# Kernel optimization log

Hardware: AMD Instinct MI355X
Metric: run time of the kernel (lower is better)

## Reference

```python
import math
import jax, jax.numpy as jnp
import numpy as np

B, S, H = 2, 2048, 2048
N_HEADS, N_KV_HEADS = 16, 4
HEAD_DIM = H // N_HEADS  # 128
ROPE_BASE = 10000.0


def setup_inputs() -> dict:
    key = jax.random.key(0)
    ks = jax.random.split(key, 8)
    hidden_states = jax.random.normal(ks[0], (B, S, H), dtype=jnp.float32)
    # continuous, increasing timestamps in [0, S)
    time_values = jnp.sort(jax.random.uniform(ks[1], (B, S), dtype=jnp.float32) * S, axis=-1)
    sc = 1.0 / math.sqrt(H)
    wq = jax.random.normal(ks[2], (H, N_HEADS * HEAD_DIM), dtype=jnp.float32) * sc
    bq = jnp.zeros((N_HEADS * HEAD_DIM,), dtype=jnp.float32)
    wk = jax.random.normal(ks[3], (H, N_KV_HEADS * HEAD_DIM), dtype=jnp.float32) * sc
    bk = jnp.zeros((N_KV_HEADS * HEAD_DIM,), dtype=jnp.float32)
    wv = jax.random.normal(ks[4], (H, N_KV_HEADS * HEAD_DIM), dtype=jnp.float32) * sc
    bv = jnp.zeros((N_KV_HEADS * HEAD_DIM,), dtype=jnp.float32)
    wo = jax.random.normal(ks[5], (N_HEADS * HEAD_DIM, H), dtype=jnp.float32) * sc
    # learnable per-dimension frequency modulation (init ones, as in module)
    rope_w = jnp.ones((HEAD_DIM // 2,), dtype=jnp.float32)
    return {"hidden_states": hidden_states, "time_values": time_values,
            "wq": wq, "bq": bq, "wk": wk, "bk": bk, "wv": wv, "bv": bv,
            "wo": wo, "rope_w": rope_w}


def _rotate_half(x):
    x1, x2 = jnp.split(x, 2, axis=-1)
    return jnp.concatenate((-x2, x1), axis=-1)


def reference(hidden_states, time_values, wq, bq, wk, bk, wv, bv, wo, rope_w):
    b, s, h = hidden_states.shape
    # QKV projections -> [b, heads, s, head_dim]
    q = (hidden_states @ wq + bq).reshape(b, s, N_HEADS, HEAD_DIM).transpose(0, 2, 1, 3)
    k = (hidden_states @ wk + bk).reshape(b, s, N_KV_HEADS, HEAD_DIM).transpose(0, 2, 1, 3)
    v = (hidden_states @ wv + bv).reshape(b, s, N_KV_HEADS, HEAD_DIM).transpose(0, 2, 1, 3)
    # Continuous-time RoPE: freqs = t * inv_freq * w  -> [b, s, hd/2]
    inv_freq = 1.0 / (ROPE_BASE ** (jnp.arange(0, HEAD_DIM, 2, dtype=jnp.float32) / HEAD_DIM))
    freqs = time_values[:, :, None] * inv_freq * rope_w
    emb = jnp.concatenate((freqs, freqs), axis=-1)[:, None]  # [b, 1, s, hd]
    cos = jnp.cos(emb).astype(q.dtype)
    sin = jnp.sin(emb).astype(q.dtype)
    q = q * cos + _rotate_half(q) * sin
    k = k * cos + _rotate_half(k) * sin
    # GQA: repeat_kv
    n_rep = N_HEADS // N_KV_HEADS
    k = jnp.repeat(k, n_rep, axis=1)
    v = jnp.repeat(v, n_rep, axis=1)
    # scaled dot-product attention, causal
    scale = 1.0 / math.sqrt(HEAD_DIM)
    scores = jnp.einsum('bhqd,bhkd->bhqk', q, k) * scale
    causal = jnp.tril(jnp.ones((s, s), dtype=bool))
    scores = jnp.where(causal, scores, jnp.finfo(scores.dtype).min)
    attn = jax.nn.softmax(scores, axis=-1)
    out = jnp.einsum('bhqk,bhkd->bhqd', attn, v)  # [b, nh, s, hd]
    out = out.transpose(0, 2, 1, 3).reshape(b, s, N_HEADS * HEAD_DIM)
    return out @ wo
```

## Files before the change

### kernel.cpp

```cpp
#include <hip/hip_runtime.h>


#define S_LEN 2048
#define BATCH 2
#define NH    16
#define NKV   4
#define HD    128

typedef float  f32x4  __attribute__((ext_vector_type(4)));
typedef __bf16 bf16x8 __attribute__((ext_vector_type(8)));
typedef __bf16 bf16x4 __attribute__((ext_vector_type(4)));
typedef unsigned int u32x4 __attribute__((ext_vector_type(4)));
typedef unsigned int u32x2 __attribute__((ext_vector_type(2)));

__device__ inline unsigned short f2bf(float f) {
    unsigned u = __builtin_bit_cast(unsigned, f);
    unsigned r = (u + 0x7fffu + ((u >> 16) & 1u)) >> 16;
    return (unsigned short)r;
}

__device__ inline void gload_lds16(const void* g, void* l) {
    __builtin_amdgcn_global_load_lds(
        (const __attribute__((address_space(1))) unsigned int*)g,
        (__attribute__((address_space(3))) unsigned int*)l, 16, 0, 0);
}

__global__ void transpose_qkv(const float* __restrict__ wq,
                              const float* __restrict__ wk,
                              const float* __restrict__ wv,
                              unsigned short* __restrict__ Wt) {
    int z = blockIdx.z;
    const float* src = (z == 0) ? wq : ((z == 1) ? wk : wv);
    int C = (z == 0) ? 2048 : 512;
    long doff = (z == 0) ? 0L : ((z == 1) ? 2048L * 2048 : 2560L * 2048);
    int bx = blockIdx.x * 32, by = blockIdx.y * 32;
    if (bx >= C) return;
    __shared__ unsigned short t[32][33];
    int x = threadIdx.x, y0 = threadIdx.y;
    #pragma unroll
    for (int i = 0; i < 4; i++) {
        int y = y0 + i * 8;
        t[y][x] = f2bf(src[(long)(by + y) * C + bx + x]);
    }
    __syncthreads();
    #pragma unroll
    for (int i = 0; i < 4; i++) {
        int y = y0 + i * 8;
        Wt[doff + (long)(bx + y) * 2048 + by + x] = t[x][y];
    }
}

__global__ void transpose_to_bf16(const float* __restrict__ src,
                                  unsigned short* __restrict__ dst,
                                  int R, int C, long dst_off, int ldd) {
    __shared__ unsigned short t[32][33];
    int bx = blockIdx.x * 32, by = blockIdx.y * 32;
    int x = threadIdx.x, y0 = threadIdx.y;
    #pragma unroll
    for (int i = 0; i < 4; i++) {
        int y = y0 + i * 8;
        t[y][x] = f2bf(src[(long)(by + y) * C + bx + x]);
    }
    __syncthreads();
    #pragma unroll
    for (int i = 0; i < 4; i++) {
        int y = y0 + i * 8;
        dst[dst_off + (long)(bx + y) * ldd + by + x] = t[x][y];
    }
}

__global__ __launch_bounds__(256) void prep_kernel(
        const float* __restrict__ X, unsigned short* __restrict__ Xb,
        const float* __restrict__ bq, const float* __restrict__ bk,
        const float* __restrict__ bv, float* __restrict__ bsf,
        const float* __restrict__ tv, const float* __restrict__ rw,
        unsigned int* __restrict__ Tab) {
    int bi = blockIdx.x, tid = threadIdx.x;
    long i = ((long)bi * 256 + tid) * 8;
    {
        f32x4 a = *(const f32x4*)&X[i];
        f32x4 b = *(const f32x4*)&X[i + 4];
        u32x4 r;
        r.x = (unsigned)f2bf(a[0]) | ((unsigned)f2bf(a[1]) << 16);
        r.y = (unsigned)f2bf(a[2]) | ((unsigned)f2bf(a[3]) << 16);
        r.z = (unsigned)f2bf(b[0]) | ((unsigned)f2bf(b[1]) << 16);
        r.w = (unsigned)f2bf(b[2]) | ((unsigned)f2bf(b[3]) << 16);
        *(u32x4*)&Xb[i] = r;
    }
    if (bi < 12) {
        int ib = bi * 256 + tid;
        bsf[ib] = (ib < 2048) ? bq[ib] : ((ib < 2560) ? bk[ib - 2048] : bv[ib - 2560]);
    }
    if (bi < 1024) {
        int m = bi * 4 + (tid >> 6);
        int fi = tid & 63;
        float t = tv[m];
        float f = t * powf(10000.f, -(float)fi / 64.f) * rw[fi];
        Tab[m * 64 + fi] = (unsigned)f2bf(cosf(f)) | ((unsigned)f2bf(sinf(f)) << 16);
    }
}

__device__ __forceinline__ void stage_half(const unsigned short* __restrict__ G,
        int baseRow, long kc, unsigned short* slot, int r0, int c0, int tid) {
    gload_lds16(&G[(long)(baseRow + r0) * 2048 + kc + c0], &slot[tid * 8]);
    gload_lds16(&G[(long)(baseRow + r0 + 128) * 2048 + kc + c0], &slot[4096 + tid * 8]);
}

#define STG_A(buf, ks, kt) \
    stage_half(A,  m0, (long)(kt) * 64 + (ks) * 32, &sm[(buf) * 16384 + (ks) * 8192], r0s, c0s, tid)
#define STG_B(buf, ks, kt) \
    stage_half(Bt, n0, (long)(kt) * 64 + (ks) * 32, &sm[32768 + (buf) * 16384 + (ks) * 8192], r0s, c0s, tid)

#define NOPV ((void)0)
#define VM6  asm volatile("s_waitcnt vmcnt(6)" ::: "memory")

#define PH(buf, ks, mh, RDB, STG, VM)                                          \
    {                                                                          \
        const int sb_ = (buf) * 16384 + (ks) * 8192;                           \
        bf16x8 a0 = *(const bf16x8*)&sm[sb_ + abase + (mh) * 2048];            \
        bf16x8 a1 = *(const bf16x8*)&sm[sb_ + abase + (mh) * 2048 + 512];      \
        bf16x8 a2 = *(const bf16x8*)&sm[sb_ + abase + (mh) * 2048 + 1024];     \
        bf16x8 a3 = *(const bf16x8*)&sm[sb_ + abase + (mh) * 2048 + 1536];     \
        if (RDB) {                                                             \
            b0 = *(const bf16x8*)&sm[sb_ + bbase];                             \
            b1 = *(const bf16x8*)&sm[sb_ + bbase + 512];                       \
            b2 = *(const bf16x8*)&sm[sb_ + bbase + 1024];                      \
            b3 = *(const bf16x8*)&sm[sb_ + bbase + 1536];                      \
        }                                                                      \
        STG;                                                                   \
        VM;                                                                    \
        __builtin_amdgcn_s_barrier();                                          \
        asm volatile("s_waitcnt lgkmcnt(0)" ::: "memory");                     \
        __builtin_amdgcn_sched_barrier(0);                                     \
        __builtin_amdgcn_s_setprio(1);                                         \
        _Pragma("unroll") for (int mi = 0; mi < 4; ++mi) {                     \
            bf16x8 am = (mi == 0) ? a0 : (mi == 1) ? a1 : (mi == 2) ? a2 : a3; \
            acc[(mh) * 4 + mi][0] = __builtin_amdgcn_mfma_f32_16x16x32_bf16(   \
                am, b0, acc[(mh) * 4 + mi][0], 0, 0, 0);                       \
            acc[(mh) * 4 + mi][1] = __builtin_amdgcn_mfma_f32_16x16x32_bf16(   \
                am, b1, acc[(mh) * 4 + mi][1], 0, 0, 0);                       \
            acc[(mh) * 4 + mi][2] = __builtin_amdgcn_mfma_f32_16x16x32_bf16(   \
                am, b2, acc[(mh) * 4 + mi][2], 0, 0, 0);                       \
            acc[(mh) * 4 + mi][3] = __builtin_amdgcn_mfma_f32_16x16x32_bf16(   \
                am, b3, acc[(mh) * 4 + mi][3], 0, 0, 0);                       \
        }                                                                      \
        __builtin_amdgcn_s_setprio(0);                                         \
        __builtin_amdgcn_s_barrier();                                          \
    }

#define GEMM_PRO_LOOP(NIT)                                                     \
    STG_B(0, 0, 0); STG_A(0, 0, 0); STG_B(0, 1, 0); STG_A(0, 1, 0);            \
    STG_B(1, 0, 1); STG_A(1, 0, 1); STG_B(1, 1, 1);                            \
    asm volatile("s_waitcnt vmcnt(6)" ::: "memory");                           \
    __builtin_amdgcn_s_barrier();                                              \
    for (int it = 0; it < (NIT); ++it) {                                       \
        const int t1  = 2 * it + 1;                                            \
        const int tn0 = (it < (NIT) - 1) ? 2 * it + 2 : 2 * (NIT) - 1;         \
        const int tn1 = (it < (NIT) - 1) ? 2 * it + 3 : 2 * (NIT) - 1;         \
        PH(0, 0, 0, 1, STG_A(1, 1, t1),  NOPV);                                \
        PH(0, 0, 1, 0, STG_B(0, 0, tn0), NOPV);                                \
        PH(0, 1, 0, 1, STG_A(0, 0, tn0), NOPV);                                \
        PH(0, 1, 1, 0, STG_B(0, 1, tn0), VM6);                                 \
        PH(1, 0, 0, 1, STG_A(0, 1, tn0), NOPV);                                \
        PH(1, 0, 1, 0, STG_B(1, 0, tn1), NOPV);                                \
        PH(1, 1, 0, 1, STG_A(1, 0, tn1), NOPV);                                \
        PH(1, 1, 1, 0, STG_B(1, 1, tn1), VM6);                                 \
    }

__global__ __launch_bounds__(512, 2) void gemm_qkv_rope(
        const unsigned short* __restrict__ A,
        const unsigned short* __restrict__ Bt,
        const float* __restrict__ bsf,
        const unsigned int* __restrict__ Tab,
        unsigned short* __restrict__ Qr,
        unsigned short* __restrict__ Kr,
        unsigned short* __restrict__ Vt) {
    __shared__ __align__(16) unsigned short sm[65536];

    const int tid = threadIdx.x;
    const int wid = tid >> 6, lane = tid & 63, quad = lane >> 4, l16 = lane & 15;
    const int wr = wid >> 2, wc = wid & 3;

    const int u   = blockIdx.y * 12 + blockIdx.x;
    const int swz = (u & 7) * 24 + (u >> 3);
    const int bx  = swz % 12;
    const int m0  = (swz / 12) * 256;
    const int n0  = bx * 256;

    const int sg    = (quad ^ ((l16 >> 1) & 3)) * 8;
    const int abase = wr * 4096 + l16 * 32 + sg;
    const int bbase = 32768 + wc * 2048 + l16 * 32 + sg;

    const int r0s = tid >> 2;
    const int c0s = ((tid & 3) ^ ((r0s >> 1) & 3)) * 8;

    f32x4 acc[8][4];
    #pragma unroll
    for (int i = 0; i < 8; i++)
        #pragma unroll
        for (int j = 0; j < 4; j++)
            #pragma unroll
            for (int c = 0; c < 4; c++) acc[i][j][c] = 0.f;
    bf16x8 b0 = {}, b1 = {}, b2 = {}, b3 = {};

    GEMM_PRO_LOOP(16)

    asm volatile("s_waitcnt vmcnt(0)" ::: "memory");
    __syncthreads();

    float* Ep = (float*)sm;
    const int EPLD = 264;
    float bv4[4];
    #pragma unroll
    for (int ni = 0; ni < 4; ++ni) bv4[ni] = bsf[n0 + wc * 64 + ni * 16 + l16];
    const bool isV = (bx >= 10);
    const float qs = (bx < 8) ? (0.08838834764831845f * 1.4426950408889634f) : 1.0f;

    const int lt = tid >> 4, hh = (tid >> 3) & 1, jj = tid & 7, j0 = jj * 8;
    const int vd = tid >> 1, vsh = tid & 1;

    #pragma unroll
    for (int p = 0; p < 8; ++p) {
        if (wr == (p >> 2)) {
            #pragma unroll
            for (int f = 0; f < 2; ++f) {
                #pragma unroll
                for (int ni = 0; ni < 4; ++ni)
                    #pragma unroll
                    for (int r = 0; r < 4; ++r)
                        Ep[(f * 16 + quad * 4 + r) * EPLD + wc * 64 + ni * 16 + l16] =
                            acc[(p & 3) * 2 + f][ni][r] + bv4[ni];
            }
        }
        __syncthreads();
        if (!isV) {
            const int gm = m0 + p * 32 + lt;
            const int bb = gm >> 11, s = gm & 2047;
            unsigned short* dst = (bx < 8)
                ? Qr + ((long)(bb * NH + bx * 2 + hh) * S_LEN + s) * HD
                : Kr + ((long)(bb * NKV + (bx - 8) * 2 + hh) * S_LEN + s) * HD;
            u32x4 t0 = *(const u32x4*)&Tab[(long)gm * 64 + j0];
            u32x4 t1v = *(const u32x4*)&Tab[(long)gm * 64 + j0 + 4];
            f32x4 x1a = *(f32x4*)&Ep[lt * EPLD + hh * 128 + j0];
            f32x4 x1b = *(f32x4*)&Ep[lt * EPLD + hh * 128 + j0 + 4];
            f32x4 x2a = *(f32x4*)&Ep[lt * EPLD + hh * 128 + 64 + j0];
            f32x4 x2b = *(f32x4*)&Ep[lt * EPLD + hh * 128 + 64 + j0 + 4];
            f32x4 la, lb, ha, hb;
            #pragma unroll
            for (int e = 0; e < 4; e++) {
                float ca = __builtin_bit_cast(float, t0[e] << 16);
                float sa = __builtin_bit_cast(float, t0[e] & 0xffff0000u);
                float cb = __builtin_bit_cast(float, t1v[e] << 16);
                float sbv = __builtin_bit_cast(float, t1v[e] & 0xffff0000u);
                la[e] = (x1a[e] * ca - x2a[e] * sa) * qs;
                ha[e] = (x2a[e] * ca + x1a[e] * sa) * qs;
                lb[e] = (x1b[e] * cb - x2b[e] * sbv) * qs;
                hb[e] = (x2b[e] * cb + x1b[e] * sbv) * qs;
            }
            u32x4 lo, hi;
            lo.x = (unsigned)f2bf(la[0]) | ((unsigned)f2bf(la[1]) << 16);
            lo.y = (unsigned)f2bf(la[2]) | ((unsigned)f2bf(la[3]) << 16);
            lo.z = (unsigned)f2bf(lb[0]) | ((unsigned)f2bf(lb[1]) << 16);
            lo.w = (unsigned)f2bf(lb[2]) | ((unsigned)f2bf(lb[3]) << 16);
            hi.x = (unsigned)f2bf(ha[0]) | ((unsigned)f2bf(ha[1]) << 16);
            hi.y = (unsigned)f2bf(ha[2]) | ((unsigned)f2bf(ha[3]) << 16);
            hi.z = (unsigned)f2bf(hb[0]) | ((unsigned)f2bf(hb[1]) << 16);
            hi.w = (unsigned)f2bf(hb[2]) | ((unsigned)f2bf(hb[3]) << 16);
            *(u32x4*)&dst[j0] = lo;
            *(u32x4*)&dst[64 + j0] = hi;
        } else {
            const int gmb = m0 + p * 32 + vsh * 16;
            const int bb = gmb >> 11, s0 = gmb & 2047;
            const int vh = (bx - 10) * 2 + (vd >> 7), dl = vd & 127;
            unsigned short* dst = Vt + ((long)(bb * NKV + vh) * HD + dl) * S_LEN + s0;
            unsigned short pv[16];
            #pragma unroll
            for (int t = 0; t < 16; ++t)
                pv[t] = f2bf(Ep[(vsh * 16 + t) * EPLD + vd]);
            u32x4 v0, v1;
            v0.x = (unsigned)pv[0]  | ((unsigned)pv[1]  << 16);
            v0.y = (unsigned)pv[2]  | ((unsigned)pv[3]  << 16);
            v0.z = (unsigned)pv[4]  | ((unsigned)pv[5]  << 16);
            v0.w = (unsigned)pv[6]  | ((unsigned)pv[7]  << 16);
            v1.x = (unsigned)pv[8]  | ((unsigned)pv[9]  << 16);
            v1.y = (unsigned)pv[10] | ((unsigned)pv[11] << 16);
            v1.z = (unsigned)pv[12] | ((unsigned)pv[13] << 16);
            v1.w = (unsigned)pv[14] | ((unsigned)pv[15] << 16);
            *(u32x4*)&dst[0] = v0;
            *(u32x4*)&dst[8] = v1;
        }
        __syncthreads();
    }
}

template <typename CT>
__global__ __launch_bounds__(256) void gemm_bt_async(
        const unsigned short* __restrict__ A,
        const unsigned short* __restrict__ Bt,
        CT* __restrict__ C,
        const float* __restrict__ bias,
        int K, int lda, int ldb, int ldc) {
    __shared__ __align__(16) unsigned short As[128 * 64];
    __shared__ __align__(16) unsigned short Bs[128 * 64];
    const int tid = threadIdx.x;
    const int wid = tid >> 6, lane = tid & 63, quad = lane >> 4, l16 = lane & 15;
    const int wr = wid >> 1, wc = wid & 1;
    const int m0 = blockIdx.y * 128, n0 = blockIdx.x * 128;
    const int l7 = l16 & 7;

    f32x4 acc[4][4];
    #pragma unroll
    for (int i = 0; i < 4; i++)
        #pragma unroll
        for (int j = 0; j < 4; j++)
            #pragma unroll
            for (int c = 0; c < 4; c++) acc[i][j][c] = 0.f;

    for (int k0 = 0; k0 < K; k0 += 64) {
        #pragma unroll
        for (int i = 0; i < 4; i++) {
            int c = tid + 256 * i;
            int row = c >> 3, loct = ((c & 7) ^ (row & 7)) * 8;
            gload_lds16(&A[(long)(m0 + row) * lda + k0 + loct], &As[c * 8]);
        }
        #pragma unroll
        for (int i = 0; i < 4; i++) {
            int c = tid + 256 * i;
            int row = c >> 3, loct = ((c & 7) ^ (row & 7)) * 8;
            gload_lds16(&Bt[(long)(n0 + row) * ldb + k0 + loct], &Bs[c * 8]);
        }
        __syncthreads();
        #pragma unroll
        for (int s = 0; s < 2; s++) {
            bf16x8 af[4], bfr[4];
            #pragma unroll
            for (int mi = 0; mi < 4; mi++)
                af[mi] = *(const bf16x8*)
                    &As[(wr * 64 + mi * 16 + l16) * 64 + (((s * 4 + quad) ^ l7)) * 8];
            #pragma unroll
            for (int ni = 0; ni < 4; ni++)
                bfr[ni] = *(const bf16x8*)
                    &Bs[(wc * 64 + ni * 16 + l16) * 64 + (((s * 4 + quad) ^ l7)) * 8];
            #pragma unroll
            for (int mi = 0; mi < 4; mi++)
                #pragma unroll
                for (int ni = 0; ni < 4; ni++)
                    acc[mi][ni] = __builtin_amdgcn_mfma_f32_16x16x32_bf16(
                        af[mi], bfr[ni], acc[mi][ni], 0, 0, 0);
        }
        __syncthreads();
    }

    #pragma unroll
    for (int mi = 0; mi < 4; mi++) {
        #pragma unroll
        for (int ni = 0; ni < 4; ni++) {
            int gn = n0 + wc * 64 + ni * 16 + l16;
            float bv_ = bias ? bias[gn] : 0.f;
            #pragma unroll
            for (int r = 0; r < 4; r++) {
                int gm = m0 + wr * 64 + mi * 16 + quad * 4 + r;
                float v = acc[mi][ni][r] + bv_;
                if constexpr (sizeof(CT) == 4) C[(long)gm * ldc + gn] = v;
                else                           C[(long)gm * ldc + gn] = f2bf(v);
            }
        }
    }
}

__global__ __launch_bounds__(512, 4) void attn_kernel(
        const unsigned short* __restrict__ Qr,
        const unsigned short* __restrict__ Kr,
        const unsigned short* __restrict__ Vt,
        unsigned short* __restrict__ Out) {
    __shared__ __align__(16) unsigned short Ks[64 * 128];
    __shared__ __align__(16) unsigned short Vs[128 * 64];
    __shared__ __align__(16) unsigned short Ps[8][16 * 68];

    const int x = blockIdx.x, y = blockIdx.y;
    const int hk = x & 3, b = (x >> 2) & 1;
    const int h  = ((x & 3) << 2) + (x >> 3);
    const int qt = (y < 8) ? y : 23 - y;
    const int tid = threadIdx.x, w = tid >> 6, lane = tid & 63;
    const int quad = lane >> 4, l16 = lane & 15;
    const unsigned short* Qb = Qr + (long)((b * NH + h) * S_LEN) * HD;
    const unsigned short* Kb = Kr + (long)((b * NKV + hk) * S_LEN) * HD;
    const unsigned short* Vb = Vt + (long)((b * NKV + hk) * HD) * S_LEN;
    const int qw = qt * 128 + w * 16;
    const int q  = qw + l16;
    const float MASK_MIN = -3.0e38f;

    bf16x8 qf[4];
    #pragma unroll
    for (int kc = 0; kc < 4; kc++)
        qf[kc] = *(const bf16x8*)&Qb[(long)q * HD + kc * 32 + quad * 8];

    f32x4 o[8];
    #pragma unroll
    for (int db = 0; db < 8; db++)
        #pragma unroll
        for (int c = 0; c < 4; c++) o[db][c] = 0.f;
    float mr = MASK_MIN, lr = 0.f;

    const int sK0 = tid, sK1 = tid + 512;
    const int kR0 = sK0 >> 4, kC0 = ((sK0 & 15) ^ (kR0 & 15)) * 8;
    const int kR1 = sK1 >> 4, kC1 = ((sK1 & 15) ^ (kR1 & 15)) * 8;
    const int vR0 = sK0 >> 3, vC0 = ((sK0 & 7) ^ (vR0 & 7)) * 8;
    const int vR1 = sK1 >> 3, vC1 = ((sK1 & 7) ^ (vR1 & 7)) * 8;

    const int nkt = 2 * qt + 2;
    for (int kt = 0; kt < nkt; kt++) {
        const int k0 = kt * 64;
        __syncthreads();
        gload_lds16(&Kb[(long)(k0 + kR0) * HD + kC0], &Ks[sK0 * 8]);
        gload_lds16(&Kb[(long)(k0 + kR1) * HD + kC1], &Ks[sK1 * 8]);
        gload_lds16(&Vb[(long)vR0 * S_LEN + k0 + vC0], &Vs[sK0 * 8]);
        gload_lds16(&Vb[(long)vR1 * S_LEN + k0 + vC1], &Vs[sK1 * 8]);
        __syncthreads();

        if (k0 > qw + 15) continue;

        f32x4 sc[4];
        #pragma unroll
        for (int nb = 0; nb < 4; nb++) {
            #pragma unroll
            for (int c = 0; c < 4; c++) sc[nb][c] = 0.f;
            #pragma unroll
            for (int kc = 0; kc < 4; kc++) {
                bf16x8 kf = *(const bf16x8*)
                    &Ks[(nb * 16 + l16) * 128 + (((kc * 4 + quad) ^ l16) * 8)];
                sc[nb] = __builtin_amdgcn_mfma_f32_16x16x32_bf16(kf, qf[kc], sc[nb], 0, 0, 0);
            }
        }
        if (k0 + 63 > qw) {
            #pragma unroll
            for (int nb = 0; nb < 4; nb++) {
                int kvb = k0 + nb * 16 + quad * 4;
                #pragma unroll
                for (int r = 0; r < 4; r++)
                    sc[nb][r] = (kvb + r > q) ? MASK_MIN : sc[nb][r];
            }
        }
        float tm = MASK_MIN;
        #pragma unroll
        for (int nb = 0; nb < 4; nb++)
            #pragma unroll
            for (int r = 0; r < 4; r++) tm = fmaxf(tm, sc[nb][r]);
        tm = fmaxf(tm, __shfl_xor(tm, 16));
        tm = fmaxf(tm, __shfl_xor(tm, 32));

        float mn = mr;
        if (__any(tm > mr + 8.f)) {
            mn = fmaxf(mr, tm);
            float alpha = exp2f(mr - mn);
            mr = mn;
            lr *= alpha;
            #pragma unroll
            for (int db = 0; db < 8; db++)
                #pragma unroll
                for (int c = 0; c < 4; c++) o[db][c] *= alpha;
        }
        float rs = 0.f;
        #pragma unroll
        for (int nb = 0; nb < 4; nb++) {
            float pv0 = exp2f(sc[nb][0] - mn), pv1 = exp2f(sc[nb][1] - mn);
            float pv2 = exp2f(sc[nb][2] - mn), pv3 = exp2f(sc[nb][3] - mn);
            rs += (pv0 + pv1) + (pv2 + pv3);
            bf16x4 pk4 = { (__bf16)pv0, (__bf16)pv1, (__bf16)pv2, (__bf16)pv3 };
            *(bf16x4*)&Ps[w][l16 * 68 + nb * 16 + quad * 4] = pk4;
        }
        rs += __shfl_xor(rs, 16);
        rs += __shfl_xor(rs, 32);
        lr += rs;

        #pragma unroll
        for (int kk = 0; kk < 2; kk++) {
            bf16x8 pf = *(const bf16x8*)&Ps[w][l16 * 68 + kk * 32 + quad * 8];
            #pragma unroll
            for (int db = 0; db < 8; db++) {
                bf16x8 vf = *(const bf16x8*)
                    &Vs[(db * 16 + l16) * 64 + (((kk * 4 + quad) ^ (l16 & 7)) * 8)];
                o[db] = __builtin_amdgcn_mfma_f32_16x16x32_bf16(vf, pf, o[db], 0, 0, 0);
            }
        }
    }

    float inv_l = 1.0f / lr;
    long obase = (long)(b * S_LEN + q) * 2048 + h * 128 + quad * 4;
    #pragma unroll
    for (int db = 0; db < 8; db++) {
        bf16x4 pk4 = { (__bf16)(o[db][0] * inv_l), (__bf16)(o[db][1] * inv_l),
                       (__bf16)(o[db][2] * inv_l), (__bf16)(o[db][3] * inv_l) };
        *(bf16x4*)&Out[obase + db * 16] = pk4;
    }
}

extern "C" void kernel_launch(void* const* d_in, const int* in_sizes, int n_in,
                              void* d_out, int out_size, void* d_ws, size_t ws_size,
                              hipStream_t stream) {
    const float* X  = (const float*)d_in[0];
    const float* tv = (const float*)d_in[1];
    const float* wq = (const float*)d_in[2];
    const float* bq = (const float*)d_in[3];
    const float* wk = (const float*)d_in[4];
    const float* bk = (const float*)d_in[5];
    const float* wv = (const float*)d_in[6];
    const float* bv = (const float*)d_in[7];
    const float* wo = (const float*)d_in[8];
    const float* rw = (const float*)d_in[9];

    char* ws = (char*)d_ws;
    unsigned short* Wt  = (unsigned short*)ws; ws += 3072L * 2048 * 2;
    float*          bsf = (float*)ws;          ws += 3072L * 4;
    unsigned int*   Tab = (unsigned int*)ws;   ws += 4096L * 64 * 4;
    unsigned short* Qr  = (unsigned short*)ws; ws += (long)BATCH * NH  * S_LEN * HD * 2;
    unsigned short* Kr  = (unsigned short*)ws; ws += (long)BATCH * NKV * S_LEN * HD * 2;
    unsigned short* Vt  = (unsigned short*)ws; ws += (long)BATCH * NKV * HD * S_LEN * 2;
    unsigned short* AO  = (unsigned short*)ws; ws += 4096L * 2048 * 2;
    unsigned short* Xb  = AO;

    transpose_qkv<<<dim3(64, 64, 3), dim3(32, 8), 0, stream>>>(wq, wk, wv, Wt);
    prep_kernel<<<4096, 256, 0, stream>>>(X, Xb, bq, bk, bv, bsf, tv, rw, Tab);
    gemm_qkv_rope<<<dim3(12, 16), 512, 0, stream>>>(Xb, Wt, bsf, Tab, Qr, Kr, Vt);
    transpose_to_bf16<<<dim3(64, 64), dim3(32, 8), 0, stream>>>(wo, Wt, 2048, 2048, 0L, 2048);
    attn_kernel<<<dim3(32, 16, 1), 512, 0, stream>>>(Qr, Kr, Vt, AO);
    gemm_bt_async<float><<<dim3(16, 32), 256, 0, stream>>>(
        AO, Wt, (float*)d_out, nullptr, 2048, 2048, 2048, 2048);
}
```

Baseline: 299.8 us.

## Double-buffer K/V tiles in attention and reorder query-tile schedule

The attention kernel now keeps two LDS buffers for K and V, prefetching the next 64-key tile with global_load_lds while computing on the current one, and drops one of the two barriers per iteration. The P scratch buffer is changed from padded rows to an XOR-swizzled layout, and the query-tile mapping is changed so the heaviest causal tiles are launched first. This doubles K/V LDS usage, which may reduce the number of resident blocks per CU. The prefetch relies on the end-of-iteration barrier to make the loads visible without an explicit vmcnt wait.

Result: no change. 301.1 us (+0.4%).

```diff
diff --git a/kernel.cpp b/kernel.cpp
--- a/kernel.cpp
+++ b/kernel.cpp
@@ -373,14 +373,14 @@
         const unsigned short* __restrict__ Kr,
         const unsigned short* __restrict__ Vt,
         unsigned short* __restrict__ Out) {
-    __shared__ __align__(16) unsigned short Ks[64 * 128];
-    __shared__ __align__(16) unsigned short Vs[128 * 64];
-    __shared__ __align__(16) unsigned short Ps[8][16 * 68];
+    __shared__ __align__(16) unsigned short Ks[2][64 * 128];
+    __shared__ __align__(16) unsigned short Vs[2][128 * 64];
+    __shared__ __align__(16) unsigned short Ps[8][1024];
 
     const int x = blockIdx.x, y = blockIdx.y;
     const int hk = x & 3, b = (x >> 2) & 1;
     const int h  = ((x & 3) << 2) + (x >> 3);
-    const int qt = (y < 8) ? y : 23 - y;
+    const int qt = (y < 8) ? (15 - y) : (y - 8);
     const int tid = threadIdx.x, w = tid >> 6, lane = tid & 63;
     const int quad = lane >> 4, l16 = lane & 15;
     const unsigned short* Qb = Qr + (long)((b * NH + h) * S_LEN) * HD;
@@ -389,6 +389,7 @@
     const int qw = qt * 128 + w * 16;
     const int q  = qw + l16;
     const float MASK_MIN = -3.0e38f;
+    const int pswz = (l16 & 7) << 3;
 
     bf16x8 qf[4];
     #pragma unroll
@@ -409,80 +410,92 @@
     const int vR1 = sK1 >> 3, vC1 = ((sK1 & 7) ^ (vR1 & 7)) * 8;
 
     const int nkt = 2 * qt + 2;
+
+    gload_lds16(&Kb[(long)kR0 * HD + kC0], &Ks[0][sK0 * 8]);
+    gload_lds16(&Kb[(long)kR1 * HD + kC1], &Ks[0][sK1 * 8]);
+    gload_lds16(&Vb[(long)vR0 * S_LEN + vC0], &Vs[0][sK0 * 8]);
+    gload_lds16(&Vb[(long)vR1 * S_LEN + vC1], &Vs[0][sK1 * 8]);
+    __syncthreads();
+
+    int cur = 0;
     for (int kt = 0; kt < nkt; kt++) {
         const int k0 = kt * 64;
+        if (kt + 1 < nkt) {
+            const int kn = k0 + 64;
+            gload_lds16(&Kb[(long)(kn + kR0) * HD + kC0], &Ks[cur ^ 1][sK0 * 8]);
+            gload_lds16(&Kb[(long)(kn + kR1) * HD + kC1], &Ks[cur ^ 1][sK1 * 8]);
+            gload_lds16(&Vb[(long)vR0 * S_LEN + kn + vC0], &Vs[cur ^ 1][sK0 * 8]);
+            gload_lds16(&Vb[(long)vR1 * S_LEN + kn + vC1], &Vs[cur ^ 1][sK1 * 8]);
+        }
+
+        if (k0 <= qw + 15) {
+            f32x4 sc[4];
+            #pragma unroll
+            for (int nb = 0; nb < 4; nb++) {
+                #pragma unroll
+                for (int c = 0; c < 4; c++) sc[nb][c] = 0.f;
+                #pragma unroll
+                for (int kc = 0; kc < 4; kc++) {
+                    bf16x8 kf = *(const bf16x8*)
+                        &Ks[cur][(nb * 16 + l16) * 128 + (((kc * 4 + quad) ^ l16) * 8)];
+                    sc[nb] = __builtin_amdgcn_mfma_f32_16x16x32_bf16(kf, qf[kc], sc[nb], 0, 0, 0);
+                }
+            }
+            if (k0 + 63 > qw) {
+                #pragma unroll
+                for (int nb = 0; nb < 4; nb++) {
+                    int kvb = k0 + nb * 16 + quad * 4;
+                    #pragma unroll
+                    for (int r = 0; r < 4; r++)
+                        sc[nb][r] = (kvb + r > q) ? MASK_MIN : sc[nb][r];
+                }
+            }
+            float tm = MASK_MIN;
+            #pragma unroll
+            for (int nb = 0; nb < 4; nb++)
+                #pragma unroll
+                for (int r = 0; r < 4; r++) tm = fmaxf(tm, sc[nb][r]);
+            tm = fmaxf(tm, __shfl_xor(tm, 16));
+            tm = fmaxf(tm, __shfl_xor(tm, 32));
+
+            float mn = mr;
+            if (__any(tm > mr + 8.f)) {
+                mn = fmaxf(mr, tm);
+                float alpha = exp2f(mr - mn);
+                mr = mn;
+                lr *= alpha;
+                #pragma unroll
+                for (int db = 0; db < 8; db++)
+                    #pragma unroll
+                    for (int c = 0; c < 4; c++) o[db][c] *= alpha;
+            }
+            float rs = 0.f;
+            #pragma unroll
+            for (int nb = 0; nb < 4; nb++) {
+                float pv0 = exp2f(sc[nb][0] - mn), pv1 = exp2f(sc[nb][1] - mn);
+                float pv2 = exp2f(sc[nb][2] - mn), pv3 = exp2f(sc[nb][3] - mn);
+                rs += (pv0 + pv1) + (pv2 + pv3);
+                bf16x4 pk4 = { (__bf16)pv0, (__bf16)pv1, (__bf16)pv2, (__bf16)pv3 };
+                *(bf16x4*)&Ps[w][(l16 * 64 + nb * 16 + quad * 4) ^ pswz] = pk4;
+            }
+            rs += __shfl_xor(rs, 16);
+            rs += __shfl_xor(rs, 32);
+            lr += rs;
+
+            #pragma unroll
+            for (int kk = 0; kk < 2; kk++) {
+                bf16x8 pf = *(const bf16x8*)&Ps[w][(l16 * 64 + kk * 32 + quad * 8) ^ pswz];
+                #pragma unroll
+                for (int db = 0; db < 8; db++) {
+                    bf16x8 vf = *(const bf16x8*)
+                        &Vs[cur][(db * 16 + l16) * 64 + (((kk * 4 + quad) ^ (l16 & 7)) * 8)];
+                    o[db] = __builtin_amdgcn_mfma_f32_16x16x32_bf16(vf, pf, o[db], 0, 0, 0);
+                }
+            }
+        }
+
         __syncthreads();
-        gload_lds16(&Kb[(long)(k0 + kR0) * HD + kC0], &Ks[sK0 * 8]);
-        gload_lds16(&Kb[(long)(k0 + kR1) * HD + kC1], &Ks[sK1 * 8]);
-        gload_lds16(&Vb[(long)vR0 * S_LEN + k0 + vC0], &Vs[sK0 * 8]);
-        gload_lds16(&Vb[(long)vR1 * S_LEN + k0 + vC1], &Vs[sK1 * 8]);
-        __syncthreads();
-
-        if (k0 > qw + 15) continue;
-
-        f32x4 sc[4];
-        #pragma unroll
-        for (int nb = 0; nb < 4; nb++) {
-            #pragma unroll
-            for (int c = 0; c < 4; c++) sc[nb][c] = 0.f;
-            #pragma unroll
-            for (int kc = 0; kc < 4; kc++) {
-                bf16x8 kf = *(const bf16x8*)
-                    &Ks[(nb * 16 + l16) * 128 + (((kc * 4 + quad) ^ l16) * 8)];
-                sc[nb] = __builtin_amdgcn_mfma_f32_16x16x32_bf16(kf, qf[kc], sc[nb], 0, 0, 0);
-            }
-        }
-        if (k0 + 63 > qw) {
-            #pragma unroll
-            for (int nb = 0; nb < 4; nb++) {
-                int kvb = k0 + nb * 16 + quad * 4;
-                #pragma unroll
-                for (int r = 0; r < 4; r++)
-                    sc[nb][r] = (kvb + r > q) ? MASK_MIN : sc[nb][r];
-            }
-        }
-        float tm = MASK_MIN;
-        #pragma unroll
-        for (int nb = 0; nb < 4; nb++)
-            #pragma unroll
-            for (int r = 0; r < 4; r++) tm = fmaxf(tm, sc[nb][r]);
-        tm = fmaxf(tm, __shfl_xor(tm, 16));
-        tm = fmaxf(tm, __shfl_xor(tm, 32));
-
-        float mn = mr;
-        if (__any(tm > mr + 8.f)) {
-            mn = fmaxf(mr, tm);
-            float alpha = exp2f(mr - mn);
-            mr = mn;
-            lr *= alpha;
-            #pragma unroll
-            for (int db = 0; db < 8; db++)
-                #pragma unroll
-                for (int c = 0; c < 4; c++) o[db][c] *= alpha;
-        }
-        float rs = 0.f;
-        #pragma unroll
-        for (int nb = 0; nb < 4; nb++) {
-            float pv0 = exp2f(sc[nb][0] - mn), pv1 = exp2f(sc[nb][1] - mn);
-            float pv2 = exp2f(sc[nb][2] - mn), pv3 = exp2f(sc[nb][3] - mn);
-            rs += (pv0 + pv1) + (pv2 + pv3);
-            bf16x4 pk4 = { (__bf16)pv0, (__bf16)pv1, (__bf16)pv2, (__bf16)pv3 };
-            *(bf16x4*)&Ps[w][l16 * 68 + nb * 16 + quad * 4] = pk4;
-        }
-        rs += __shfl_xor(rs, 16);
-        rs += __shfl_xor(rs, 32);
-        lr += rs;
-
-        #pragma unroll
-        for (int kk = 0; kk < 2; kk++) {
-            bf16x8 pf = *(const bf16x8*)&Ps[w][l16 * 68 + kk * 32 + quad * 8];
-            #pragma unroll
-            for (int db = 0; db < 8; db++) {
-                bf16x8 vf = *(const bf16x8*)
-                    &Vs[(db * 16 + l16) * 64 + (((kk * 4 + quad) ^ (l16 & 7)) * 8)];
-                o[db] = __builtin_amdgcn_mfma_f32_16x16x32_bf16(vf, pf, o[db], 0, 0, 0);
-            }
-        }
+        cur ^= 1;
     }
 
     float inv_l = 1.0f / lr;
```

## Process two 16-row query tiles per wave in attention to reuse K/V fragments

Applied to the files above, without the earlier changes.

Attention blocks shrink from 8 to 4 waves, and each wave now owns 32 query rows as two 16-row MFMA tiles. Each K and V fragment read from LDS feeds two MFMAs, halving LDS fragment traffic per unit of compute. The cost is doubled accumulator and softmax state per wave, which raises register pressure. Fewer waves per block, with launch bounds lowered to 2 blocks per unit, may leave less latency hiding.

Result: slower. 308.4 us (+2.9%).

```diff
diff --git a/kernel.cpp b/kernel.cpp
--- a/kernel.cpp
+++ b/kernel.cpp
@@ -368,7 +368,7 @@
     }
 }
 
-__global__ __launch_bounds__(512, 4) void attn_kernel(
+__global__ __launch_bounds__(256, 2) void attn_kernel(
         const unsigned short* __restrict__ Qr,
         const unsigned short* __restrict__ Kr,
         const unsigned short* __restrict__ Vt,
@@ -386,112 +386,129 @@
     const unsigned short* Qb = Qr + (long)((b * NH + h) * S_LEN) * HD;
     const unsigned short* Kb = Kr + (long)((b * NKV + hk) * S_LEN) * HD;
     const unsigned short* Vb = Vt + (long)((b * NKV + hk) * HD) * S_LEN;
-    const int qw = qt * 128 + w * 16;
-    const int q  = qw + l16;
+    const int qw0 = qt * 128 + w * 32;
     const float MASK_MIN = -3.0e38f;
 
-    bf16x8 qf[4];
-    #pragma unroll
-    for (int kc = 0; kc < 4; kc++)
-        qf[kc] = *(const bf16x8*)&Qb[(long)q * HD + kc * 32 + quad * 8];
-
-    f32x4 o[8];
-    #pragma unroll
-    for (int db = 0; db < 8; db++)
-        #pragma unroll
-        for (int c = 0; c < 4; c++) o[db][c] = 0.f;
-    float mr = MASK_MIN, lr = 0.f;
-
-    const int sK0 = tid, sK1 = tid + 512;
-    const int kR0 = sK0 >> 4, kC0 = ((sK0 & 15) ^ (kR0 & 15)) * 8;
-    const int kR1 = sK1 >> 4, kC1 = ((sK1 & 15) ^ (kR1 & 15)) * 8;
-    const int vR0 = sK0 >> 3, vC0 = ((sK0 & 7) ^ (vR0 & 7)) * 8;
-    const int vR1 = sK1 >> 3, vC1 = ((sK1 & 7) ^ (vR1 & 7)) * 8;
+    bf16x8 qf[2][4];
+    #pragma unroll
+    for (int m = 0; m < 2; m++)
+        #pragma unroll
+        for (int kc = 0; kc < 4; kc++)
+            qf[m][kc] = *(const bf16x8*)
+                &Qb[(long)(qw0 + m * 16 + l16) * HD + kc * 32 + quad * 8];
+
+    f32x4 o[2][8];
+    #pragma unroll
+    for (int m = 0; m < 2; m++)
+        #pragma unroll
+        for (int db = 0; db < 8; db++)
+            #pragma unroll
+            for (int c = 0; c < 4; c++) o[m][db][c] = 0.f;
+    float mr[2] = { MASK_MIN, MASK_MIN }, lr[2] = { 0.f, 0.f };
 
     const int nkt = 2 * qt + 2;
     for (int kt = 0; kt < nkt; kt++) {
         const int k0 = kt * 64;
         __syncthreads();
-        gload_lds16(&Kb[(long)(k0 + kR0) * HD + kC0], &Ks[sK0 * 8]);
-        gload_lds16(&Kb[(long)(k0 + kR1) * HD + kC1], &Ks[sK1 * 8]);
-        gload_lds16(&Vb[(long)vR0 * S_LEN + k0 + vC0], &Vs[sK0 * 8]);
-        gload_lds16(&Vb[(long)vR1 * S_LEN + k0 + vC1], &Vs[sK1 * 8]);
+        #pragma unroll
+        for (int i = 0; i < 4; i++) {
+            const int s = tid + 256 * i;
+            const int kR = s >> 4, kC = ((s & 15) ^ (kR & 15)) * 8;
+            const int vR = s >> 3, vC = ((s & 7) ^ (vR & 7)) * 8;
+            gload_lds16(&Kb[(long)(k0 + kR) * HD + kC], &Ks[s * 8]);
+            gload_lds16(&Vb[(long)vR * S_LEN + k0 + vC], &Vs[s * 8]);
+        }
         __syncthreads();
 
-        if (k0 > qw + 15) continue;
-
-        f32x4 sc[4];
-        #pragma unroll
-        for (int nb = 0; nb < 4; nb++) {
-            #pragma unroll
-            for (int c = 0; c < 4; c++) sc[nb][c] = 0.f;
+        if (k0 > qw0 + 31) continue;
+
+        f32x4 sc[2][4];
+        #pragma unroll
+        for (int m = 0; m < 2; m++)
+            #pragma unroll
+            for (int nb = 0; nb < 4; nb++)
+                #pragma unroll
+                for (int c = 0; c < 4; c++) sc[m][nb][c] = 0.f;
+
+        #pragma unroll
+        for (int nb = 0; nb < 4; nb++)
             #pragma unroll
             for (int kc = 0; kc < 4; kc++) {
                 bf16x8 kf = *(const bf16x8*)
                     &Ks[(nb * 16 + l16) * 128 + (((kc * 4 + quad) ^ l16) * 8)];
-                sc[nb] = __builtin_amdgcn_mfma_f32_16x16x32_bf16(kf, qf[kc], sc[nb], 0, 0, 0);
-            }
-        }
-        if (k0 + 63 > qw) {
+                sc[0][nb] = __builtin_amdgcn_mfma_f32_16x16x32_bf16(kf, qf[0][kc], sc[0][nb], 0, 0, 0);
+                sc[1][nb] = __builtin_amdgcn_mfma_f32_16x16x32_bf16(kf, qf[1][kc], sc[1][nb], 0, 0, 0);
+            }
+
+        #pragma unroll
+        for (int m = 0; m < 2; m++) {
+            const int qwm = qw0 + m * 16, qm = qwm + l16;
+            if (k0 + 63 > qwm) {
+                #pragma unroll
+                for (int nb = 0; nb < 4; nb++) {
+                    int kvb = k0 + nb * 16 + quad * 4;
+                    #pragma unroll
+                    for (int r = 0; r < 4; r++)
+                        sc[m][nb][r] = (kvb + r > qm) ? MASK_MIN : sc[m][nb][r];
+                }
+            }
+            float tm = MASK_MIN;
+            #pragma unroll
+            for (int nb = 0; nb < 4; nb++)
+                #pragma unroll
+                for (int r = 0; r < 4; r++) tm = fmaxf(tm, sc[m][nb][r]);
+            tm = fmaxf(tm, __shfl_xor(tm, 16));
+            tm = fmaxf(tm, __shfl_xor(tm, 32));
+
+            float mn = mr[m];
+            if (__any(tm > mr[m] + 8.f)) {
+                mn = fmaxf(mr[m], tm);
+                float alpha = exp2f(mr[m] - mn);
+                mr[m] = mn;
+                lr[m] *= alpha;
+                #pragma unroll
+                for (int db = 0; db < 8; db++)
+                    #pragma unroll
+                    for (int c = 0; c < 4; c++) o[m][db][c] *= alpha;
+            }
+            float rs = 0.f;
             #pragma unroll
             for (int nb = 0; nb < 4; nb++) {
-                int kvb = k0 + nb * 16 + quad * 4;
-                #pragma unroll
-                for (int r = 0; r < 4; r++)
-                    sc[nb][r] = (kvb + r > q) ? MASK_MIN : sc[nb][r];
-            }
-        }
-        float tm = MASK_MIN;
-        #pragma unroll
-        for (int nb = 0; nb < 4; nb++)
-            #pragma unroll
-            for (int r = 0; r < 4; r++) tm = fmaxf(tm, sc[nb][r]);
-        tm = fmaxf(tm, __shfl_xor(tm, 16));
-        tm = fmaxf(tm, __shfl_xor(tm, 32));
-
-        float mn = mr;
-        if (__any(tm > mr + 8.f)) {
-            mn = fmaxf(mr, tm);
-            float alpha = exp2f(mr - mn);
-            mr = mn;
-            lr *= alpha;
-            #pragma unroll
-            for (int db = 0; db < 8; db++)
-                #pragma unroll
-                for (int c = 0; c < 4; c++) o[db][c] *= alpha;
-        }
-        float rs = 0.f;
-        #pragma unroll
-        for (int nb = 0; nb < 4; nb++) {
-            float pv0 = exp2f(sc[nb][0] - mn), pv1 = exp2f(sc[nb][1] - mn);
-            float pv2 = exp2f(sc[nb][2] - mn), pv3 = exp2f(sc[nb][3] - mn);
-            rs += (pv0 + pv1) + (pv2 + pv3);
-            bf16x4 pk4 = { (__bf16)pv0, (__bf16)pv1, (__bf16)pv2, (__bf16)pv3 };
-            *(bf16x4*)&Ps[w][l16 * 68 + nb * 16 + quad * 4] = pk4;
-        }
-        rs += __shfl_xor(rs, 16);
-        rs += __shfl_xor(rs, 32);
-        lr += rs;
+                float pv0 = exp2f(sc[m][nb][0] - mn), pv1 = exp2f(sc[m][nb][1] - mn);
+                float pv2 = exp2f(sc[m][nb][2] - mn), pv3 = exp2f(sc[m][nb][3] - mn);
+                rs += (pv0 + pv1) + (pv2 + pv3);
+                bf16x4 pk4 = { (__bf16)pv0, (__bf16)pv1, (__bf16)pv2, (__bf16)pv3 };
+                *(bf16x4*)&Ps[w * 2 + m][l16 * 68 + nb * 16 + quad * 4] = pk4;
+            }
+            rs += __shfl_xor(rs, 16);
+            rs += __shfl_xor(rs, 32);
+            lr[m] += rs;
+        }
 
         #pragma unroll
         for (int kk = 0; kk < 2; kk++) {
-            bf16x8 pf = *(const bf16x8*)&Ps[w][l16 * 68 + kk * 32 + quad * 8];
+            bf16x8 pf0 = *(const bf16x8*)&Ps[w * 2 + 0][l16 * 68 + kk * 32 + quad * 8];
+            bf16x8 pf1 = *(const bf16x8*)&Ps[w * 2 + 1][l16 * 68 + kk * 32 + quad * 8];
             #pragma unroll
             for (int db = 0; db < 8; db++) {
                 bf16x8 vf = *(const bf16x8*)
                     &Vs[(db * 16 + l16) * 64 + (((kk * 4 + quad) ^ (l16 & 7)) * 8)];
-                o[db] = __builtin_amdgcn_mfma_f32_16x16x32_bf16(vf, pf, o[db], 0, 0, 0);
-            }
-        }
-    }
-
-    float inv_l = 1.0f / lr;
-    long obase = (long)(b * S_LEN + q) * 2048 + h * 128 + quad * 4;
-    #pragma unroll
-    for (int db = 0; db < 8; db++) {
-        bf16x4 pk4 = { (__bf16)(o[db][0] * inv_l), (__bf16)(o[db][1] * inv_l),
-                       (__bf16)(o[db][2] * inv_l), (__bf16)(o[db][3] * inv_l) };
-        *(bf16x4*)&Out[obase + db * 16] = pk4;
+                o[0][db] = __builtin_amdgcn_mfma_f32_16x16x32_bf16(vf, pf0, o[0][db], 0, 0, 0);
+                o[1][db] = __builtin_amdgcn_mfma_f32_16x16x32_bf16(vf, pf1, o[1][db], 0, 0, 0);
+            }
+        }
+    }
+
+    #pragma unroll
+    for (int m = 0; m < 2; m++) {
+        float inv_l = 1.0f / lr[m];
+        long obase = (long)(b * S_LEN + qw0 + m * 16 + l16) * 2048 + h * 128 + quad * 4;
+        #pragma unroll
+        for (int db = 0; db < 8; db++) {
+            bf16x4 pk4 = { (__bf16)(o[m][db][0] * inv_l), (__bf16)(o[m][db][1] * inv_l),
+                           (__bf16)(o[m][db][2] * inv_l), (__bf16)(o[m][db][3] * inv_l) };
+            *(bf16x4*)&Out[obase + db * 16] = pk4;
+        }
     }
 }
 
@@ -523,7 +540,7 @@
     prep_kernel<<<4096, 256, 0, stream>>>(X, Xb, bq, bk, bv, bsf, tv, rw, Tab);
     gemm_qkv_rope<<<dim3(12, 16), 512, 0, stream>>>(Xb, Wt, bsf, Tab, Qr, Kr, Vt);
     transpose_to_bf16<<<dim3(64, 64), dim3(32, 8), 0, stream>>>(wo, Wt, 2048, 2048, 0L, 2048);
-    attn_kernel<<<dim3(32, 16, 1), 512, 0, stream>>>(Qr, Kr, Vt, AO);
+    attn_kernel<<<dim3(32, 16, 1), 256, 0, stream>>>(Qr, Kr, Vt, AO);
     gemm_bt_async<float><<<dim3(16, 32), 256, 0, stream>>>(
         AO, Wt, (float*)d_out, nullptr, 2048, 2048, 2048, 2048);
 }
```

## Replace output-projection GEMM with pipelined 128x256 multi-buffered kernel

Applied to the files above, without the earlier changes.

Replaces the generic synchronous output-projection GEMM with a specialized kernel that uses 512 threads, 128x256 tiles, and a four-stage LDS ring of half-K slices. Each stage issues the next asynchronous global-to-LDS loads before running its MFMAs, with fine-grained vmcnt waits and setprio. Block indices are swizzled for L2 locality. This aims to hide load latency behind compute, at the cost of more LDS per block (96KB) and more complex hand scheduling.

New measurement: 301.3 us. Within noise of the previous version (+0.5%).

```diff
diff --git a/kernel.cpp b/kernel.cpp
--- a/kernel.cpp
+++ b/kernel.cpp
@@ -293,20 +293,66 @@
     }
 }
 
-template <typename CT>
-__global__ __launch_bounds__(256) void gemm_bt_async(
+#define OSTG_A(buf, ks, kt)                                                    \
+    gload_lds16(&A[(long)(m0 + r0s) * 2048 + (kt) * 64 + (ks) * 32 + c0s],     \
+                &sm[((buf) * 2 + (ks)) * 4096 + tid * 8])
+#define OSTG_B(buf, ks, kt)                                                    \
+    stage_half(Bt, n0, (long)(kt) * 64 + (ks) * 32,                            \
+               &sm[16384 + ((buf) * 2 + (ks)) * 8192], r0s, c0s, tid)
+
+#define OPH(buf, ks, STG)                                                      \
+    {                                                                          \
+        const int ab_ = ((buf) * 2 + (ks)) * 4096 + abase;                     \
+        const int bb_ = ((buf) * 2 + (ks)) * 8192 + bbase;                     \
+        bf16x8 a0 = *(const bf16x8*)&sm[ab_];                                  \
+        bf16x8 a1 = *(const bf16x8*)&sm[ab_ + 512];                            \
+        bf16x8 a2 = *(const bf16x8*)&sm[ab_ + 1024];                           \
+        bf16x8 a3 = *(const bf16x8*)&sm[ab_ + 1536];                           \
+        bf16x8 b0 = *(const bf16x8*)&sm[bb_];                                  \
+        bf16x8 b1 = *(const bf16x8*)&sm[bb_ + 512];                            \
+        bf16x8 b2 = *(const bf16x8*)&sm[bb_ + 1024];                           \
+        bf16x8 b3 = *(const bf16x8*)&sm[bb_ + 1536];                           \
+        STG;                                                                   \
+        asm volatile("s_waitcnt vmcnt(6)" ::: "memory");                       \
+        __builtin_amdgcn_s_barrier();                                          \
+        asm volatile("s_waitcnt lgkmcnt(0)" ::: "memory");                     \
+        __builtin_amdgcn_sched_barrier(0);                                     \
+        __builtin_amdgcn_s_setprio(1);                                         \
+        _Pragma("unroll") for (int mi = 0; mi < 4; ++mi) {                     \
+            bf16x8 am = (mi == 0) ? a0 : (mi == 1) ? a1 : (mi == 2) ? a2 : a3; \
+            acc[mi][0] = __builtin_amdgcn_mfma_f32_16x16x32_bf16(              \
+                am, b0, acc[mi][0], 0, 0, 0);                                  \
+            acc[mi][1] = __builtin_amdgcn_mfma_f32_16x16x32_bf16(              \
+                am, b1, acc[mi][1], 0, 0, 0);                                  \
+            acc[mi][2] = __builtin_amdgcn_mfma_f32_16x16x32_bf16(              \
+                am, b2, acc[mi][2], 0, 0, 0);                                  \
+            acc[mi][3] = __builtin_amdgcn_mfma_f32_16x16x32_bf16(              \
+                am, b3, acc[mi][3], 0, 0, 0);                                  \
+        }                                                                      \
+        __builtin_amdgcn_s_setprio(0);                                         \
+        __builtin_amdgcn_s_barrier();                                          \
+    }
+
+__global__ __launch_bounds__(512, 2) void gemm_o(
         const unsigned short* __restrict__ A,
         const unsigned short* __restrict__ Bt,
-        CT* __restrict__ C,
-        const float* __restrict__ bias,
-        int K, int lda, int ldb, int ldc) {
-    __shared__ __align__(16) unsigned short As[128 * 64];
-    __shared__ __align__(16) unsigned short Bs[128 * 64];
+        float* __restrict__ C) {
+    __shared__ __align__(16) unsigned short sm[49152];
+
     const int tid = threadIdx.x;
     const int wid = tid >> 6, lane = tid & 63, quad = lane >> 4, l16 = lane & 15;
-    const int wr = wid >> 1, wc = wid & 1;
-    const int m0 = blockIdx.y * 128, n0 = blockIdx.x * 128;
-    const int l7 = l16 & 7;
+    const int wr = wid >> 2, wc = wid & 3;
+
+    const int u   = blockIdx.y * 8 + blockIdx.x;
+    const int swz = (u & 7) * 32 + (u >> 3);
+    const int m0  = (swz & 31) * 128;
+    const int n0  = (swz >> 5) * 256;
+
+    const int sg    = (quad ^ ((l16 >> 1) & 3)) * 8;
+    const int abase = (wr * 64 + l16) * 32 + sg;
+    const int bbase = 16384 + (wc * 64 + l16) * 32 + sg;
+    const int r0s = tid >> 2;
+    const int c0s = ((tid & 3) ^ ((r0s >> 1) & 3)) * 8;
 
     f32x4 acc[4][4];
     #pragma unroll
@@ -316,56 +362,35 @@
             #pragma unroll
             for (int c = 0; c < 4; c++) acc[i][j][c] = 0.f;
 
-    for (int k0 = 0; k0 < K; k0 += 64) {
-        #pragma unroll
-        for (int i = 0; i < 4; i++) {
-            int c = tid + 256 * i;
-            int row = c >> 3, loct = ((c & 7) ^ (row & 7)) * 8;
-            gload_lds16(&A[(long)(m0 + row) * lda + k0 + loct], &As[c * 8]);
-        }
-        #pragma unroll
-        for (int i = 0; i < 4; i++) {
-            int c = tid + 256 * i;
-            int row = c >> 3, loct = ((c & 7) ^ (row & 7)) * 8;
-            gload_lds16(&Bt[(long)(n0 + row) * ldb + k0 + loct], &Bs[c * 8]);
-        }
-        __syncthreads();
-        #pragma unroll
-        for (int s = 0; s < 2; s++) {
-            bf16x8 af[4], bfr[4];
-            #pragma unroll
-            for (int mi = 0; mi < 4; mi++)
-                af[mi] = *(const bf16x8*)
-                    &As[(wr * 64 + mi * 16 + l16) * 64 + (((s * 4 + quad) ^ l7)) * 8];
-            #pragma unroll
-            for (int ni = 0; ni < 4; ni++)
-                bfr[ni] = *(const bf16x8*)
-                    &Bs[(wc * 64 + ni * 16 + l16) * 64 + (((s * 4 + quad) ^ l7)) * 8];
-            #pragma unroll
-            for (int mi = 0; mi < 4; mi++)
-                #pragma unroll
-                for (int ni = 0; ni < 4; ni++)
-                    acc[mi][ni] = __builtin_amdgcn_mfma_f32_16x16x32_bf16(
-                        af[mi], bfr[ni], acc[mi][ni], 0, 0, 0);
-        }
-        __syncthreads();
-    }
-
-    #pragma unroll
-    for (int mi = 0; mi < 4; mi++) {
+    OSTG_A(0, 0, 0); OSTG_B(0, 0, 0);
+    OSTG_A(0, 1, 0); OSTG_B(0, 1, 0);
+    OSTG_A(1, 0, 1); OSTG_B(1, 0, 1);
+    asm volatile("s_waitcnt vmcnt(6)" ::: "memory");
+    __builtin_amdgcn_s_barrier();
+
+    for (int it = 0; it < 16; ++it) {
+        const int t1  = 2 * it + 1;
+        const int tn0 = (it < 15) ? 2 * it + 2 : 31;
+        const int tn1 = (it < 15) ? 2 * it + 3 : 31;
+        OPH(0, 0, OSTG_A(1, 1, t1);  OSTG_B(1, 1, t1))
+        OPH(0, 1, OSTG_A(0, 0, tn0); OSTG_B(0, 0, tn0))
+        OPH(1, 0, OSTG_A(0, 1, tn0); OSTG_B(0, 1, tn0))
+        OPH(1, 1, OSTG_A(1, 0, tn1); OSTG_B(1, 0, tn1))
+    }
+
+    asm volatile("s_waitcnt vmcnt(0)" ::: "memory");
+
+    #pragma unroll
+    for (int mi = 0; mi < 4; mi++)
         #pragma unroll
         for (int ni = 0; ni < 4; ni++) {
-            int gn = n0 + wc * 64 + ni * 16 + l16;
-            float bv_ = bias ? bias[gn] : 0.f;
+            const int gn = n0 + wc * 64 + ni * 16 + l16;
             #pragma unroll
             for (int r = 0; r < 4; r++) {
-                int gm = m0 + wr * 64 + mi * 16 + quad * 4 + r;
-                float v = acc[mi][ni][r] + bv_;
-                if constexpr (sizeof(CT) == 4) C[(long)gm * ldc + gn] = v;
-                else                           C[(long)gm * ldc + gn] = f2bf(v);
+                const int gm = m0 + wr * 64 + mi * 16 + quad * 4 + r;
+                C[(long)gm * 2048 + gn] = acc[mi][ni][r];
             }
         }
-    }
 }
 
 __global__ __launch_bounds__(512, 4) void attn_kernel(
@@ -524,6 +549,5 @@
     gemm_qkv_rope<<<dim3(12, 16), 512, 0, stream>>>(Xb, Wt, bsf, Tab, Qr, Kr, Vt);
     transpose_to_bf16<<<dim3(64, 64), dim3(32, 8), 0, stream>>>(wo, Wt, 2048, 2048, 0L, 2048);
     attn_kernel<<<dim3(32, 16, 1), 512, 0, stream>>>(Qr, Kr, Vt, AO);
-    gemm_bt_async<float><<<dim3(16, 32), 256, 0, stream>>>(
-        AO, Wt, (float*)d_out, nullptr, 2048, 2048, 2048, 2048);
-}
+    gemm_o<<<dim3(8, 32), 512, 0, stream>>>(AO, Wt, (float*)d_out);
+}
```
